# Kernel optimization log

Measured on AMD Instinct MI355X. Metric: run time of the kernel, lower is better.

## Reference

```python
import jax, jax.numpy as jnp
import numpy as np

D_MODEL = 2048
MLP = 8192
E = 8
R = 16
ALPHA = 32
SCALING = ALPHA / R  # lora_alpha / rank


def setup_inputs() -> dict:
    key = jax.random.key(0)
    ks = jax.random.split(key, 16)
    s = 0.02
    return {
        "x": jax.random.normal(ks[0], (4, 1024, D_MODEL), dtype=jnp.float32),
        # frozen base weights (nn.Linear stores [out, in])
        "w_gate": jax.random.normal(ks[1], (MLP, D_MODEL), dtype=jnp.float32) * s,
        "w_up": jax.random.normal(ks[2], (MLP, D_MODEL), dtype=jnp.float32) * s,
        "w_down": jax.random.normal(ks[3], (D_MODEL, MLP), dtype=jnp.float32) * s,
        # router
        "router_w": jax.random.normal(ks[4], (E, D_MODEL), dtype=jnp.float32) * s,
        "router_b": jnp.zeros((E,), dtype=jnp.float32),
        # LoRA expert params: A [E, r, fan_in], B [E, fan_out, r]
        "A_gate": jax.random.normal(ks[5], (E, R, D_MODEL), dtype=jnp.float32) * s,
        "B_gate": jax.random.normal(ks[6], (E, MLP, R), dtype=jnp.float32) * s,
        "A_up": jax.random.normal(ks[7], (E, R, D_MODEL), dtype=jnp.float32) * s,
        "B_up": jax.random.normal(ks[8], (E, MLP, R), dtype=jnp.float32) * s,
        "A_down": jax.random.normal(ks[9], (E, R, MLP), dtype=jnp.float32) * s,
        "B_down": jax.random.normal(ks[10], (E, D_MODEL, R), dtype=jnp.float32) * s,
    }


def _lora_moe_sparse(inp, W, A, B, onehot):
    # inp: [B,S,din], W: [dout,din], A: [E,r,din], B: [E,dout,r], onehot: [B,S,E]
    base = jnp.einsum("bsd,od->bso", inp, W)
    # low-rank projection for every expert is tiny: [B,S,E,r]
    t = jnp.einsum("bsd,erd->bser", inp, A)
    # top-1 dispatch: onehot zeroes out non-selected experts (== scatter assign,
    # since each token has exactly one expert)
    lora = jnp.einsum("bser,bse,eor->bso", t, onehot, B) * SCALING
    return base + lora


def reference(x, w_gate, w_up, w_down, router_w, router_b,
              A_gate, B_gate, A_up, B_up, A_down, B_down):
    logits = jnp.einsum("bsd,ed->bse", x, router_w) + router_b
    routing = jax.nn.softmax(logits, axis=-1)
    index = jnp.argmax(routing, axis=-1)                 # [B,S]
    y_hard = jax.nn.one_hot(index, E, dtype=logits.dtype)  # [B,S,E]
    expert_choice = y_hard - jax.lax.stop_gradient(routing) + routing

    gate_out = _lora_moe_sparse(x, w_gate, A_gate, B_gate, y_hard)
    up_out = _lora_moe_sparse(x, w_up, A_up, B_up, y_hard)
    h = jax.nn.silu(gate_out) * up_out
    out = _lora_moe_sparse(h, w_down, A_down, B_down, y_hard)
    return (out, routing, expert_choice)
```

## Files before the change

kernel.cpp:

```cpp
#include <hip/hip_runtime.h>
#include <stdint.h>

#define NTOK   4096
#define DM     2048
#define DMLP   8192
#define NEXP   8
#define NRANK  16
#define SCAL   2.0f

#define LDXA 2304
#define LDHA 8320

typedef __bf16 bf16x8 __attribute__((ext_vector_type(8)));
typedef float  f32x4  __attribute__((ext_vector_type(4)));
typedef unsigned short u16;

__device__ __forceinline__ u16 f2bf(float f) {
  unsigned u = __float_as_uint(f);
  u += 0x7fffu + ((u >> 16) & 1u);
  return (u16)(u >> 16);
}

__device__ __forceinline__ void gload_lds16(const void* g, void* l) {
  __builtin_amdgcn_global_load_lds((const __attribute__((address_space(1))) void*)g,
                                   (__attribute__((address_space(3))) void*)l, 16, 0, 0);
}

__global__ void prep_kernel(const float* __restrict__ wg, const float* __restrict__ wu,
                            const float* __restrict__ wd,
                            const float* __restrict__ Ag, const float* __restrict__ Au,
                            const float* __restrict__ Ad,
                            const float* __restrict__ Bg, const float* __restrict__ Bu,
                            const float* __restrict__ Bd,
                            u16* __restrict__ wgx, u16* __restrict__ wux,
                            u16* __restrict__ wdx, u16* __restrict__ Aab,
                            u16* __restrict__ Adb) {
  const int gt = blockIdx.x * blockDim.x + threadIdx.x;
  const int gs = gridDim.x * blockDim.x;

  for (int i = gt; i < DMLP * 512; i += gs) {
    const int o = i >> 9, c = (i & 511) << 2;
    float4 v = ((const float4*)wg)[i];
    ushort4 ov; ov.x = f2bf(v.x); ov.y = f2bf(v.y); ov.z = f2bf(v.z); ov.w = f2bf(v.w);
    *(ushort4*)(wgx + (size_t)o * LDXA + c) = ov;
    v = ((const float4*)wu)[i];
    ov.x = f2bf(v.x); ov.y = f2bf(v.y); ov.z = f2bf(v.z); ov.w = f2bf(v.w);
    *(ushort4*)(wux + (size_t)o * LDXA + c) = ov;
  }
  for (int i = gt; i < DM * 2048; i += gs) {
    const int o = i >> 11, c = (i & 2047) << 2;
    float4 v = ((const float4*)wd)[i];
    ushort4 ov; ov.x = f2bf(v.x); ov.y = f2bf(v.y); ov.z = f2bf(v.z); ov.w = f2bf(v.w);
    *(ushort4*)(wdx + (size_t)o * LDHA + c) = ov;
  }
  for (int i = gt; i < 256 * 512; i += gs) {
    float4 v = (i < 128 * 512) ? ((const float4*)Ag)[i] : ((const float4*)Au)[i - 128 * 512];
    ushort4 ov; ov.x = f2bf(v.x); ov.y = f2bf(v.y); ov.z = f2bf(v.z); ov.w = f2bf(v.w);
    ((ushort4*)Aab)[i] = ov;
  }
  for (int i = gt; i < 128 * 2048; i += gs) {
    float4 v = ((const float4*)Ad)[i];
    ushort4 ov; ov.x = f2bf(v.x); ov.y = f2bf(v.y); ov.z = f2bf(v.z); ov.w = f2bf(v.w);
    ((ushort4*)Adb)[i] = ov;
  }
  for (int i = gt; i < DMLP * 256; i += gs) {
    const int o = i >> 8, c = i & 255;
    const int e = (c & 127) >> 4, r = c & 15;
    u16 vg = 0, vu = 0;
    if (c < 128) vg = f2bf(Bg[((size_t)e * DMLP + o) * NRANK + r]);
    else         vu = f2bf(Bu[((size_t)e * DMLP + o) * NRANK + r]);
    wgx[(size_t)o * LDXA + 2048 + c] = vg;
    wux[(size_t)o * LDXA + 2048 + c] = vu;
  }
  for (int i = gt; i < DM * 128; i += gs) {
    const int o = i >> 7, c = i & 127;
    const int e = c >> 4, r = c & 15;
    wdx[(size_t)o * LDHA + 8192 + c] = f2bf(Bd[((size_t)e * DM + o) * NRANK + r]);
  }
}

__global__ void router_kernel(const float* __restrict__ x,
                              const float* __restrict__ rw,
                              const float* __restrict__ rb,
                              u16* __restrict__ xa,
                              int* __restrict__ idx,
                              float* __restrict__ out_rout,
                              float* __restrict__ out_ec) {
  const int wave = threadIdx.x >> 6;
  const int lane = threadIdx.x & 63;
  const int m = blockIdx.x * 4 + wave;

  const float4* xrow = (const float4*)(x + (size_t)m * DM + lane * 32);
  float4 xv[8];
#pragma unroll
  for (int i = 0; i < 8; ++i) xv[i] = xrow[i];

  uint4 o[4];
  unsigned* op = (unsigned*)o;
#pragma unroll
  for (int i = 0; i < 8; ++i) {
    op[2*i]   = (unsigned)f2bf(xv[i].x) | ((unsigned)f2bf(xv[i].y) << 16);
    op[2*i+1] = (unsigned)f2bf(xv[i].z) | ((unsigned)f2bf(xv[i].w) << 16);
  }
  uint4* xdst = (uint4*)(xa + (size_t)m * LDXA + lane * 32);
#pragma unroll
  for (int i = 0; i < 4; ++i) xdst[i] = o[i];

  float lg[NEXP];
#pragma unroll
  for (int e = 0; e < NEXP; ++e) {
    const float4* wrow = (const float4*)(rw + (size_t)e * DM + lane * 32);
    float s = 0.f;
#pragma unroll
    for (int i = 0; i < 8; ++i) {
      float4 wv = wrow[i];
      s += xv[i].x*wv.x + xv[i].y*wv.y + xv[i].z*wv.z + xv[i].w*wv.w;
    }
#pragma unroll
    for (int off = 32; off > 0; off >>= 1) s += __shfl_xor(s, off, 64);
    lg[e] = s + rb[e];
  }

  float mx = lg[0];
#pragma unroll
  for (int e = 1; e < NEXP; ++e) mx = fmaxf(mx, lg[e]);
  float ex[NEXP], se = 0.f;
#pragma unroll
  for (int e = 0; e < NEXP; ++e) { ex[e] = expf(lg[e] - mx); se += ex[e]; }
  float inv = 1.f / se;
  int best = 0; float bv = lg[0];
#pragma unroll
  for (int e = 1; e < NEXP; ++e) if (lg[e] > bv) { bv = lg[e]; best = e; }

  if (lane == 0) {
    idx[m] = best;
#pragma unroll
    for (int e = 0; e < NEXP; ++e) {
      float r = ex[e] * inv;
      out_rout[(size_t)m * NEXP + e] = r;
      float hard = (e == best) ? 1.f : 0.f;
      out_ec[(size_t)m * NEXP + e] = (hard - r) + r;
    }
  }
}

template<int MODE>
__global__ __launch_bounds__(256, 2)
void gemm_kernel(const u16* __restrict__ A,
                 const u16* __restrict__ B0,
                 const int* __restrict__ idx,
                 void* __restrict__ Cout)
{
  constexpr int LDA = (MODE == 0) ? LDXA : LDHA;
  constexpr int LDB = (MODE == 0) ? 2048 : 8192;
  constexpr int NKI = (MODE == 0) ? 64 : 32;

  __shared__ u16 lds[16384];

  const int tid = threadIdx.x;
  const int w = tid >> 6;
  const int l = tid & 63;
  const int wm = w >> 1, wn = w & 1;
  const int mtile = blockIdx.x;
  const int ntile = (MODE == 3) ? 0 : (int)blockIdx.y;
  const int ks    = (MODE == 3) ? (int)blockIdx.y : 0;
  const int kb0   = (MODE == 3) ? ks * 1024 : 0;

  int srow[2];
  srow[0] = w * 16 + (l >> 2);
  srow[1] = 64 + srow[0];
  const int chunk = (l & 3) ^ ((srow[0] >> 1) & 3);
  const int scol = chunk * 8;

  const u16* aptr[2];
  const u16* bptr[2];
#pragma unroll
  for (int i = 0; i < 2; ++i) {
    aptr[i] = A + (size_t)(mtile * 128 + srow[i]) * LDA + kb0 + scol;
    bptr[i] = B0 + (size_t)(ntile * 128 + srow[i]) * LDB + kb0 + scol;
  }

  char* ldsc = (char*)lds;
  auto stage = [&](int buf, int kt) {
    const int kk = kt * 32;
    char* base = ldsc + buf * 16384;
#pragma unroll
    for (int i = 0; i < 2; ++i) {
      gload_lds16(aptr[i] + kk, base + i * 4096 + w * 1024);
      gload_lds16(bptr[i] + kk, base + 8192 + i * 4096 + w * 1024);
    }
  };

  f32x4 acc[4][4];
  f32x4 zf = {0.f, 0.f, 0.f, 0.f};
#pragma unroll
  for (int a = 0; a < 4; ++a)
#pragma unroll
    for (int b = 0; b < 4; ++b) acc[a][b] = zf;

  stage(0, 0);
  __syncthreads();

  const int kq   = l >> 4;
  const int arow = wm * 64 + (l & 15);
  const int brow = wn * 64 + (l & 15);
  const int axor = (kq ^ ((arow >> 1) & 3)) << 4;
  const int bxor = (kq ^ ((brow >> 1) & 3)) << 4;

  for (int kt = 0; kt < NKI; ++kt) {
    const int buf = kt & 1;
    if (kt + 1 < NKI) stage(buf ^ 1, kt + 1);
    const char* bA = ldsc + buf * 16384;
    const char* bB = bA + 8192;
    bf16x8 af[4], bfr[4];
#pragma unroll
    for (int fm = 0; fm < 4; ++fm)
      af[fm] = *(const bf16x8*)(bA + (arow + fm * 16) * 64 + axor);
#pragma unroll
    for (int fn = 0; fn < 4; ++fn)
      bfr[fn] = *(const bf16x8*)(bB + (brow + fn * 16) * 64 + bxor);
#pragma unroll
    for (int fm = 0; fm < 4; ++fm)
#pragma unroll
      for (int fn = 0; fn < 4; ++fn)
        acc[fm][fn] = __builtin_amdgcn_mfma_f32_16x16x32_bf16(af[fm], bfr[fn], acc[fm][fn], 0, 0, 0);
    __syncthreads();
  }

  const int lq = l >> 4;
  const int lr = l & 15;

  if (MODE == 0) {
    u16* X = (u16*)Cout;
#pragma unroll
    for (int fm = 0; fm < 4; ++fm)
#pragma unroll
      for (int fn = 0; fn < 4; ++fn)
        for (int j = 0; j < 4; ++j) {
          int m = mtile * 128 + wm * 64 + fm * 16 + lq * 4 + j;
          int c = ntile * 128 + wn * 64 + fn * 16 + lr;
          int e = idx[m];
          u16 v = (((c & 127) >> 4) == e) ? f2bf(SCAL * acc[fm][fn][j]) : (u16)0;
          X[(size_t)m * LDXA + 2048 + c] = v;
        }
  } else {
    float* P = (float*)Cout + (size_t)ks * NTOK * 128;
#pragma unroll
    for (int fm = 0; fm < 4; ++fm)
#pragma unroll
      for (int fn = 0; fn < 4; ++fn)
        for (int j = 0; j < 4; ++j) {
          int m = mtile * 128 + wm * 64 + fm * 16 + lq * 4 + j;
          int c = wn * 64 + fn * 16 + lr;
          P[(size_t)m * 128 + c] = acc[fm][fn][j];
        }
  }
}

__global__ __launch_bounds__(512, 2)
void gemm_gu(const u16* __restrict__ Ag,
             const u16* __restrict__ B0g,
             const u16* __restrict__ B1g,
             u16* __restrict__ H)
{
  constexpr int NKT = 36;
  __shared__ char L[131072];

  const int tid = threadIdx.x, w = tid >> 6, l = tid & 63;
  const int wm = w >> 2, wn = w & 3;
  const int bid = blockIdx.x;
  const int rr = bid >> 3;
  const int mtile = rr >> 3;
  const int ntile = (bid & 7) * 8 + (rr & 7);

  const u16 *agb0, *agb1, *bgb0, *bgb1;
  {
    int row0 = tid >> 2, row1 = 128 + row0;
    int lc = (tid & 3) ^ ((row0 >> 1) & 3);
    agb0 = Ag + (size_t)(mtile * 256 + row0) * LDXA + lc * 8;
    agb1 = Ag + (size_t)(mtile * 256 + row1) * LDXA + lc * 8;
    int c0 = ntile * 128 + ((row0 >> 5) << 4) + (row0 & 15);
    int c1 = ntile * 128 + ((row1 >> 5) << 4) + (row1 & 15);
    bgb0 = (((row0 >> 4) & 1) ? B1g : B0g) + (size_t)c0 * LDXA + lc * 8;
    bgb1 = (((row1 >> 4) & 1) ? B1g : B0g) + (size_t)c1 * LDXA + lc * 8;
  }
  const int sdst = w * 1024;

#define STGA(z, kt) { const int ko_ = ((kt) < NKT ? (kt) : NKT - 1) * 64 + ((z) & 1) * 32; \
    gload_lds16(agb0 + ko_, L + (z) * 16384 + sdst); \
    gload_lds16(agb1 + ko_, L + (z) * 16384 + 8192 + sdst); }
#define STGB(z, kt) { const int ko_ = ((kt) < NKT ? (kt) : NKT - 1) * 64 + ((z) & 1) * 32; \
    gload_lds16(bgb0 + ko_, L + 65536 + (z) * 16384 + sdst); \
    gload_lds16(bgb1 + ko_, L + 65536 + (z) * 16384 + 8192 + sdst); }

  const int lr = l & 15;
  const int kob = (((l >> 4) ^ ((lr >> 1) & 3)) << 4);
  const int abase = (wm * 128 + lr) * 64 + kob;
  const int bbase = (wn * 64 + lr) * 64 + kob;

  bf16x8 A0_[4], A1_[4], B0_[4], B1_[4];
#define RDA(S, z, qa) _Pragma("unroll") for (int f = 0; f < 4; ++f) \
    S[f] = *(const bf16x8*)(L + (z) * 16384 + abase + (qa) * 4096 + f * 1024);
#define RDB(S, z) _Pragma("unroll") for (int f = 0; f < 4; ++f) \
    S[f] = *(const bf16x8*)(L + 65536 + (z) * 16384 + bbase + f * 1024);

  f32x4 acc[8][4];
  f32x4 zf = {0.f, 0.f, 0.f, 0.f};
#pragma unroll
  for (int a = 0; a < 8; ++a)
#pragma unroll
    for (int b = 0; b < 4; ++b) acc[a][b] = zf;

#define MF(qa, AS, BS) \
  __builtin_amdgcn_s_setprio(1); \
  _Pragma("unroll") for (int f = 0; f < 4; ++f) \
    _Pragma("unroll") for (int n = 0; n < 4; ++n) \
      acc[(qa) * 4 + f][n] = __builtin_amdgcn_mfma_f32_16x16x32_bf16(AS[f], BS[n], acc[(qa) * 4 + f][n], 0, 0, 0); \
  __builtin_amdgcn_s_setprio(0);

#define VMW  { asm volatile("s_waitcnt vmcnt(6)" ::: "memory"); __builtin_amdgcn_sched_barrier(0); }
#define PEND { __builtin_amdgcn_sched_barrier(0); __builtin_amdgcn_s_barrier(); __builtin_amdgcn_sched_barrier(0); }

  STGA(0, 0) STGB(0, 0)
  STGA(1, 0) STGB(1, 0)
  STGA(2, 1) STGB(2, 1)
  VMW
  PEND
  RDB(B0_, 0) RDA(A0_, 0, 0)

  for (int it = 0; it < NKT / 2; ++it) {
    const int k1 = 2 * it + 1, k2 = 2 * it + 2, k3 = 2 * it + 3;
    STGA(3, k1)
    RDA(A1_, 0, 1)
    MF(0, A0_, B0_)  VMW  PEND
    STGB(3, k1)
    RDB(B1_, 1) RDA(A0_, 1, 0)
    MF(1, A1_, B0_)  PEND
    STGA(0, k2)
    RDA(A1_, 1, 1)
    MF(0, A0_, B1_)  VMW  PEND
    STGB(0, k2)
    RDB(B0_, 2) RDA(A0_, 2, 0)
    MF(1, A1_, B1_)  PEND
    STGA(1, k2)
    RDA(A1_, 2, 1)
    MF(0, A0_, B0_)  VMW  PEND
    STGB(1, k2)
    RDB(B1_, 3) RDA(A0_, 3, 0)
    MF(1, A1_, B0_)  PEND
    STGA(2, k3)
    RDA(A1_, 3, 1)
    MF(0, A0_, B1_)  VMW  PEND
    STGB(2, k3)
    RDB(B0_, 0) RDA(A0_, 0, 0)
    MF(1, A1_, B1_)  PEND
  }

  const int lq = l >> 4;
#pragma unroll
  for (int fm = 0; fm < 8; ++fm)
    for (int jj = 0; jj < 4; ++jj) {
      const int m = mtile * 256 + wm * 128 + fm * 16 + lq * 4 + jj;
#pragma unroll
      for (int p = 0; p < 2; ++p) {
        float g = acc[fm][2 * p][jj];
        float u = acc[fm][2 * p + 1][jj];
        float e = __builtin_amdgcn_exp2f(g * -1.44269504089f);
        float h = g * __builtin_amdgcn_rcpf(1.f + e) * u;
        const int c = ntile * 128 + (wn * 2 + p) * 16 + lr;
        H[(size_t)m * LDHA + c] = f2bf(h);
      }
    }
#undef RDA
#undef RDB
#undef MF
#undef STGA
#undef STGB
#undef VMW
#undef PEND
}

__global__ __launch_bounds__(512, 2)
void gemm6(const u16* __restrict__ Ag,
           const u16* __restrict__ Bg,
           float* __restrict__ C)
{
  __shared__ char L[147456];
  const int tid = threadIdx.x, w = tid >> 6, l = tid & 63;
  const int wm = w >> 2, wn = w & 3;
  const int bid = blockIdx.x;
  const int swz = (bid & 7) * 32 + (bid >> 3);
  const int mtile = swz >> 3;
  const int ntile = swz & 7;

  const u16 *agb0, *bgb0, *bgb1;
  {
    int row0 = tid >> 2;
    int lc = (tid & 3) ^ ((row0 >> 1) & 3);
    agb0 = Ag + (size_t)(mtile * 128 + row0) * LDHA + lc * 8;
    bgb0 = Bg + (size_t)(ntile * 256 + row0) * LDHA + lc * 8;
    bgb1 = Bg + (size_t)(ntile * 256 + 128 + row0) * LDHA + lc * 8;
  }
  const int sdst = w * 1024;

#define STG6(z, g) { const int gg_ = (g) < 260 ? (g) : 259; \
    const int ko_ = (gg_ >> 1) * 64 + (gg_ & 1) * 32; \
    gload_lds16(agb0 + ko_, L + (z) * 24576 + sdst); \
    gload_lds16(bgb0 + ko_, L + (z) * 24576 + 8192 + sdst); \
    gload_lds16(bgb1 + ko_, L + (z) * 24576 + 16384 + sdst); }

  const int lr = l & 15;
  const int kob = (((l >> 4) ^ ((lr >> 1) & 3)) << 4);
  const int abase = (wm * 64 + lr) * 64 + kob;
  const int bbase = (wn * 64 + lr) * 64 + kob;

  bf16x8 A0_[4], A1_[4], B0_[4], B1_[4];
#define RDA6(S, z) _Pragma("unroll") for (int f = 0; f < 4; ++f) \
    S[f] = *(const bf16x8*)(L + (z) * 24576 + abase + f * 1024);
#define RDB6(S, z) _Pragma("unroll") for (int f = 0; f < 4; ++f) \
    S[f] = *(const bf16x8*)(L + (z) * 24576 + 8192 + bbase + f * 1024);

  f32x4 acc[4][4];
  f32x4 zf = {0.f, 0.f, 0.f, 0.f};
#pragma unroll
  for (int a = 0; a < 4; ++a)
#pragma unroll
    for (int b = 0; b < 4; ++b) acc[a][b] = zf;

#define MF6(AS, BS) \
  __builtin_amdgcn_s_setprio(1); \
  _Pragma("unroll") for (int f = 0; f < 4; ++f) \
    _Pragma("unroll") for (int n = 0; n < 4; ++n) \
      acc[f][n] = __builtin_amdgcn_mfma_f32_16x16x32_bf16(AS[f], BS[n], acc[f][n], 0, 0, 0); \
  __builtin_amdgcn_s_setprio(0);

#define VMW6 { asm volatile("s_waitcnt vmcnt(6)" ::: "memory"); __builtin_amdgcn_sched_barrier(0); }
#define PEND6 { __builtin_amdgcn_sched_barrier(0); __builtin_amdgcn_s_barrier(); __builtin_amdgcn_sched_barrier(0); }

  STG6(0, 0) STG6(1, 1) STG6(2, 2) STG6(3, 3)
  VMW6
  PEND6
  RDB6(B0_, 0) RDA6(A0_, 0)

  for (int it = 0; it < 43; ++it) {
    const int g4 = it * 6 + 4;
    STG6(4, g4)      RDB6(B1_, 1) RDA6(A1_, 1)  MF6(A0_, B0_)  VMW6  PEND6
    STG6(5, g4 + 1)  RDB6(B0_, 2) RDA6(A0_, 2)  MF6(A1_, B1_)  VMW6  PEND6
    STG6(0, g4 + 2)  RDB6(B1_, 3) RDA6(A1_, 3)  MF6(A0_, B0_)  VMW6  PEND6
    STG6(1, g4 + 3)  RDB6(B0_, 4) RDA6(A0_, 4)  MF6(A1_, B1_)  VMW6  PEND6
    STG6(2, g4 + 4)  RDB6(B1_, 5) RDA6(A1_, 5)  MF6(A0_, B0_)  VMW6  PEND6
    STG6(3, g4 + 5)  RDB6(B0_, 0) RDA6(A0_, 0)  MF6(A1_, B1_)  VMW6  PEND6
  }
  RDB6(B1_, 1) RDA6(A1_, 1)
  MF6(A0_, B0_)
  MF6(A1_, B1_)

  const int lq = l >> 4;
#pragma unroll
  for (int fm = 0; fm < 4; ++fm)
#pragma unroll
    for (int n = 0; n < 4; ++n)
      for (int jj = 0; jj < 4; ++jj) {
        const int m = mtile * 128 + wm * 64 + fm * 16 + lq * 4 + jj;
        const int c = ntile * 256 + wn * 64 + n * 16 + lr;
        C[(size_t)m * DM + c] = acc[fm][n][jj];
      }
#undef RDA6
#undef RDB6
#undef MF6
#undef STG6
#undef VMW6
#undef PEND6
}

__global__ void td_reduce(const float* __restrict__ part,
                          const int* __restrict__ idx,
                          u16* __restrict__ ha) {
  int i = blockIdx.x * blockDim.x + threadIdx.x;
  int m = i >> 7, c = i & 127;
  float s = 0.f;
#pragma unroll
  for (int k = 0; k < 8; ++k) s += part[(size_t)k * NTOK * 128 + i];
  u16 v = ((c >> 4) == idx[m]) ? f2bf(SCAL * s) : (u16)0;
  ha[(size_t)m * LDHA + 8192 + c] = v;
}

extern "C" void kernel_launch(void* const* d_in, const int* in_sizes, int n_in,
                              void* d_out, int out_size, void* d_ws, size_t ws_size,
                              hipStream_t stream) {
  const float* x  = (const float*)d_in[0];
  const float* wg = (const float*)d_in[1];
  const float* wu = (const float*)d_in[2];
  const float* wd = (const float*)d_in[3];
  const float* rw = (const float*)d_in[4];
  const float* rb = (const float*)d_in[5];
  const float* Ag = (const float*)d_in[6];
  const float* Bg = (const float*)d_in[7];
  const float* Au = (const float*)d_in[8];
  const float* Bu = (const float*)d_in[9];
  const float* Ad = (const float*)d_in[10];
  const float* Bd = (const float*)d_in[11];

  float* out      = (float*)d_out;
  float* out_rout = out + (size_t)NTOK * DM;
  float* out_ec   = out_rout + (size_t)NTOK * NEXP;

  char* ws = (char*)d_ws;
  size_t off = 0;
  auto take = [&](size_t b) { void* p = ws + off; off += (b + 255) & ~(size_t)255; return p; };
  u16*   xa   = (u16*)take((size_t)NTOK * LDXA * 2);
  u16*   ha   = (u16*)take((size_t)NTOK * LDHA * 2);
  u16*   wgx  = (u16*)take((size_t)DMLP * LDXA * 2);
  u16*   wux  = (u16*)take((size_t)DMLP * LDXA * 2);
  u16*   wdx  = (u16*)take((size_t)DM * LDHA * 2);
  u16*   Aab  = (u16*)take((size_t)256 * DM * 2);
  u16*   Adb  = (u16*)take((size_t)128 * DMLP * 2);
  float* tdp  = (float*)take((size_t)8 * NTOK * 128 * 4);
  int*   idx  = (int*)take((size_t)NTOK * 4);
  if (off > ws_size) return;

  prep_kernel<<<2048, 256, 0, stream>>>(wg, wu, wd, Ag, Au, Ad, Bg, Bu, Bd,
                                        wgx, wux, wdx, Aab, Adb);

  router_kernel<<<NTOK / 4, 256, 0, stream>>>(x, rw, rb, xa, idx, out_rout, out_ec);

  gemm_kernel<0><<<dim3(32, 2), 256, 0, stream>>>(xa, Aab, idx, xa);
  gemm_gu<<<1024, 512, 0, stream>>>(xa, wgx, wux, ha);
  gemm_kernel<3><<<dim3(32, 8), 256, 0, stream>>>(ha, Adb, idx, tdp);
  td_reduce<<<NTOK * 128 / 256, 256, 0, stream>>>(tdp, idx, ha);
  gemm6<<<256, 512, 0, stream>>>(ha, wdx, out);
}
```

Before: 556.7 us.

## Restructure gate/up GEMM pipeline into per-slice stages with fewer barriers

The gate/up fused GEMM main loop is reorganised. It now stages A and B for a whole 32-wide k-slice together in one buffer and runs 32 MFMAs per phase, instead of splitting A and B loads across half-phases of 16 MFMAs. The aim is to halve the number of block barriers per k-step and give the scheduler larger MFMA groups to overlap with LDS reads and global loads. In exchange it uses more A fragment registers, which adds register pressure at two blocks per CU, and it changes the vmcnt wait depth.

```diff
diff --git a/kernel.cpp b/kernel.cpp
--- a/kernel.cpp
+++ b/kernel.cpp
@@ -263,7 +263,7 @@
              const u16* __restrict__ B1g,
              u16* __restrict__ H)
 {
-  constexpr int NKT = 36;
+  constexpr int NSL = 72;
   __shared__ char L[131072];
 
   const int tid = threadIdx.x, w = tid >> 6, l = tid & 63;
@@ -286,10 +286,9 @@
   }
   const int sdst = w * 1024;
 
-#define STGA(z, kt) { const int ko_ = ((kt) < NKT ? (kt) : NKT - 1) * 64 + ((z) & 1) * 32; \
+#define STG(z, s) { const int ko_ = ((s) < NSL ? (s) : NSL - 1) * 32; \
     gload_lds16(agb0 + ko_, L + (z) * 16384 + sdst); \
-    gload_lds16(agb1 + ko_, L + (z) * 16384 + 8192 + sdst); }
-#define STGB(z, kt) { const int ko_ = ((kt) < NKT ? (kt) : NKT - 1) * 64 + ((z) & 1) * 32; \
+    gload_lds16(agb1 + ko_, L + (z) * 16384 + 8192 + sdst); \
     gload_lds16(bgb0 + ko_, L + 65536 + (z) * 16384 + sdst); \
     gload_lds16(bgb1 + ko_, L + 65536 + (z) * 16384 + 8192 + sdst); }
 
@@ -298,9 +297,9 @@
   const int abase = (wm * 128 + lr) * 64 + kob;
   const int bbase = (wn * 64 + lr) * 64 + kob;
 
-  bf16x8 A0_[4], A1_[4], B0_[4], B1_[4];
-#define RDA(S, z, qa) _Pragma("unroll") for (int f = 0; f < 4; ++f) \
-    S[f] = *(const bf16x8*)(L + (z) * 16384 + abase + (qa) * 4096 + f * 1024);
+  bf16x8 A0_[8], A1_[8], B0_[4], B1_[4];
+#define RDA8(S, z) _Pragma("unroll") for (int f = 0; f < 8; ++f) \
+    S[f] = *(const bf16x8*)(L + (z) * 16384 + abase + (f >> 2) * 4096 + (f & 3) * 1024);
 #define RDB(S, z) _Pragma("unroll") for (int f = 0; f < 4; ++f) \
     S[f] = *(const bf16x8*)(L + 65536 + (z) * 16384 + bbase + f * 1024);
 
@@ -311,49 +310,35 @@
 #pragma unroll
     for (int b = 0; b < 4; ++b) acc[a][b] = zf;
 
-#define MF(qa, AS, BS) \
+#define MF32(AS, BS) \
   __builtin_amdgcn_s_setprio(1); \
-  _Pragma("unroll") for (int f = 0; f < 4; ++f) \
+  _Pragma("unroll") for (int f = 0; f < 8; ++f) \
     _Pragma("unroll") for (int n = 0; n < 4; ++n) \
-      acc[(qa) * 4 + f][n] = __builtin_amdgcn_mfma_f32_16x16x32_bf16(AS[f], BS[n], acc[(qa) * 4 + f][n], 0, 0, 0); \
+      acc[f][n] = __builtin_amdgcn_mfma_f32_16x16x32_bf16(AS[f], BS[n], acc[f][n], 0, 0, 0); \
   __builtin_amdgcn_s_setprio(0);
 
-#define VMW  { asm volatile("s_waitcnt vmcnt(6)" ::: "memory"); __builtin_amdgcn_sched_barrier(0); }
+#define VMW  { asm volatile("s_waitcnt vmcnt(4)" ::: "memory"); __builtin_amdgcn_sched_barrier(0); }
 #define PEND { __builtin_amdgcn_sched_barrier(0); __builtin_amdgcn_s_barrier(); __builtin_amdgcn_sched_barrier(0); }
 
-  STGA(0, 0) STGB(0, 0)
-  STGA(1, 0) STGB(1, 0)
-  STGA(2, 1) STGB(2, 1)
+  STG(0, 0) STG(1, 1) STG(2, 2)
   VMW
   PEND
-  RDB(B0_, 0) RDA(A0_, 0, 0)
-
-  for (int it = 0; it < NKT / 2; ++it) {
-    const int k1 = 2 * it + 1, k2 = 2 * it + 2, k3 = 2 * it + 3;
-    STGA(3, k1)
-    RDA(A1_, 0, 1)
-    MF(0, A0_, B0_)  VMW  PEND
-    STGB(3, k1)
-    RDB(B1_, 1) RDA(A0_, 1, 0)
-    MF(1, A1_, B0_)  PEND
-    STGA(0, k2)
-    RDA(A1_, 1, 1)
-    MF(0, A0_, B1_)  VMW  PEND
-    STGB(0, k2)
-    RDB(B0_, 2) RDA(A0_, 2, 0)
-    MF(1, A1_, B1_)  PEND
-    STGA(1, k2)
-    RDA(A1_, 2, 1)
-    MF(0, A0_, B0_)  VMW  PEND
-    STGB(1, k2)
-    RDB(B1_, 3) RDA(A0_, 3, 0)
-    MF(1, A1_, B0_)  PEND
-    STGA(2, k3)
-    RDA(A1_, 3, 1)
-    MF(0, A0_, B1_)  VMW  PEND
-    STGB(2, k3)
-    RDB(B0_, 0) RDA(A0_, 0, 0)
-    MF(1, A1_, B1_)  PEND
+  RDB(B0_, 0) RDA8(A0_, 0)
+
+  for (int it = 0; it < NSL / 4; ++it) {
+    const int s = 4 * it;
+    STG(3, s + 3)
+    RDB(B1_, 1) RDA8(A1_, 1)
+    MF32(A0_, B0_)  VMW  PEND
+    STG(0, s + 4)
+    RDB(B0_, 2) RDA8(A0_, 2)
+    MF32(A1_, B1_)  VMW  PEND
+    STG(1, s + 5)
+    RDB(B1_, 3) RDA8(A1_, 3)
+    MF32(A0_, B0_)  VMW  PEND
+    STG(2, s + 6)
+    RDB(B0_, 0) RDA8(A0_, 0)
+    MF32(A1_, B1_)  VMW  PEND
   }
 
   const int lq = l >> 4;
@@ -371,11 +356,10 @@
         H[(size_t)m * LDHA + c] = f2bf(h);
       }
     }
-#undef RDA
+#undef RDA8
 #undef RDB
-#undef MF
-#undef STGA
-#undef STGB
+#undef MF32
+#undef STG
 #undef VMW
 #undef PEND
 }
```

Result: slower. 604.0 us (+8.5%).

## Overlap big weight conversion with LoRA-A GEMM and merge router with small prep

Applied to the files above, without the earlier changes.

The router and the small LoRA-A conversions are merged into one kernel. The large fp32-to-bf16 conversion of the base and LoRA-B weights is moved into the same launch as the x·A GEMM: the first 64 blocks run the GEMM and the remaining blocks grid-stride over the weight conversion. This removes two launches and lets the narrow 64-block GEMM overlap with bandwidth-bound conversion work instead of leaving most CUs idle. The risk is that conversion blocks compete for bandwidth with the GEMM blocks and slow them down.

```diff
diff --git a/kernel.cpp b/kernel.cpp
--- a/kernel.cpp
+++ b/kernel.cpp
@@ -26,17 +26,190 @@
                                    (__attribute__((address_space(3))) void*)l, 16, 0, 0);
 }
 
-__global__ void prep_kernel(const float* __restrict__ wg, const float* __restrict__ wu,
-                            const float* __restrict__ wd,
-                            const float* __restrict__ Ag, const float* __restrict__ Au,
-                            const float* __restrict__ Ad,
-                            const float* __restrict__ Bg, const float* __restrict__ Bu,
-                            const float* __restrict__ Bd,
-                            u16* __restrict__ wgx, u16* __restrict__ wux,
-                            u16* __restrict__ wdx, u16* __restrict__ Aab,
-                            u16* __restrict__ Adb) {
+__global__ void prep_small(const float* __restrict__ x,
+                           const float* __restrict__ rw,
+                           const float* __restrict__ rb,
+                           u16* __restrict__ xa,
+                           int* __restrict__ idx,
+                           float* __restrict__ out_rout,
+                           float* __restrict__ out_ec,
+                           const float* __restrict__ Ag,
+                           const float* __restrict__ Au,
+                           const float* __restrict__ Ad,
+                           u16* __restrict__ Aab,
+                           u16* __restrict__ Adb) {
+  const int wave = threadIdx.x >> 6;
+  const int lane = threadIdx.x & 63;
+  const int m = blockIdx.x * 4 + wave;
+
+  const float4* xrow = (const float4*)(x + (size_t)m * DM + lane * 32);
+  float4 xv[8];
+#pragma unroll
+  for (int i = 0; i < 8; ++i) xv[i] = xrow[i];
+
+  uint4 o[4];
+  unsigned* op = (unsigned*)o;
+#pragma unroll
+  for (int i = 0; i < 8; ++i) {
+    op[2*i]   = (unsigned)f2bf(xv[i].x) | ((unsigned)f2bf(xv[i].y) << 16);
+    op[2*i+1] = (unsigned)f2bf(xv[i].z) | ((unsigned)f2bf(xv[i].w) << 16);
+  }
+  uint4* xdst = (uint4*)(xa + (size_t)m * LDXA + lane * 32);
+#pragma unroll
+  for (int i = 0; i < 4; ++i) xdst[i] = o[i];
+
+  float lg[NEXP];
+#pragma unroll
+  for (int e = 0; e < NEXP; ++e) {
+    const float4* wrow = (const float4*)(rw + (size_t)e * DM + lane * 32);
+    float s = 0.f;
+#pragma unroll
+    for (int i = 0; i < 8; ++i) {
+      float4 wv = wrow[i];
+      s += xv[i].x*wv.x + xv[i].y*wv.y + xv[i].z*wv.z + xv[i].w*wv.w;
+    }
+#pragma unroll
+    for (int off = 32; off > 0; off >>= 1) s += __shfl_xor(s, off, 64);
+    lg[e] = s + rb[e];
+  }
+
+  float mx = lg[0];
+#pragma unroll
+  for (int e = 1; e < NEXP; ++e) mx = fmaxf(mx, lg[e]);
+  float ex[NEXP], se = 0.f;
+#pragma unroll
+  for (int e = 0; e < NEXP; ++e) { ex[e] = expf(lg[e] - mx); se += ex[e]; }
+  float inv = 1.f / se;
+  int best = 0; float bv = lg[0];
+#pragma unroll
+  for (int e = 1; e < NEXP; ++e) if (lg[e] > bv) { bv = lg[e]; best = e; }
+
+  if (lane == 0) {
+    idx[m] = best;
+#pragma unroll
+    for (int e = 0; e < NEXP; ++e) {
+      float r = ex[e] * inv;
+      out_rout[(size_t)m * NEXP + e] = r;
+      float hard = (e == best) ? 1.f : 0.f;
+      out_ec[(size_t)m * NEXP + e] = (hard - r) + r;
+    }
+  }
+
   const int gt = blockIdx.x * blockDim.x + threadIdx.x;
   const int gs = gridDim.x * blockDim.x;
+  for (int i = gt; i < 256 * 512; i += gs) {
+    float4 v = (i < 128 * 512) ? ((const float4*)Ag)[i] : ((const float4*)Au)[i - 128 * 512];
+    ushort4 ov; ov.x = f2bf(v.x); ov.y = f2bf(v.y); ov.z = f2bf(v.z); ov.w = f2bf(v.w);
+    ((ushort4*)Aab)[i] = ov;
+  }
+  for (int i = gt; i < 128 * 2048; i += gs) {
+    float4 v = ((const float4*)Ad)[i];
+    ushort4 ov; ov.x = f2bf(v.x); ov.y = f2bf(v.y); ov.z = f2bf(v.z); ov.w = f2bf(v.w);
+    ((ushort4*)Adb)[i] = ov;
+  }
+}
+
+__global__ __launch_bounds__(256, 2)
+void gemm0_prep(const u16* __restrict__ A,
+                const u16* __restrict__ B0,
+                const int* __restrict__ idx,
+                u16* __restrict__ Xout,
+                const float* __restrict__ wg, const float* __restrict__ wu,
+                const float* __restrict__ wd,
+                const float* __restrict__ Bg, const float* __restrict__ Bu,
+                const float* __restrict__ Bd,
+                u16* __restrict__ wgx, u16* __restrict__ wux,
+                u16* __restrict__ wdx)
+{
+  __shared__ u16 lds[16384];
+
+  if (blockIdx.x < 64) {
+    const int tid = threadIdx.x;
+    const int w = tid >> 6;
+    const int l = tid & 63;
+    const int wm = w >> 1, wn = w & 1;
+    const int mtile = (int)blockIdx.x >> 1;
+    const int ntile = (int)blockIdx.x & 1;
+
+    int srow[2];
+    srow[0] = w * 16 + (l >> 2);
+    srow[1] = 64 + srow[0];
+    const int chunk = (l & 3) ^ ((srow[0] >> 1) & 3);
+    const int scol = chunk * 8;
+
+    const u16* aptr[2];
+    const u16* bptr[2];
+#pragma unroll
+    for (int i = 0; i < 2; ++i) {
+      aptr[i] = A + (size_t)(mtile * 128 + srow[i]) * LDXA + scol;
+      bptr[i] = B0 + (size_t)(ntile * 128 + srow[i]) * 2048 + scol;
+    }
+
+    char* ldsc = (char*)lds;
+    auto stage = [&](int buf, int kt) {
+      const int kk = kt * 32;
+      char* base = ldsc + buf * 16384;
+#pragma unroll
+      for (int i = 0; i < 2; ++i) {
+        gload_lds16(aptr[i] + kk, base + i * 4096 + w * 1024);
+        gload_lds16(bptr[i] + kk, base + 8192 + i * 4096 + w * 1024);
+      }
+    };
+
+    f32x4 acc[4][4];
+    f32x4 zf = {0.f, 0.f, 0.f, 0.f};
+#pragma unroll
+    for (int a = 0; a < 4; ++a)
+#pragma unroll
+      for (int b = 0; b < 4; ++b) acc[a][b] = zf;
+
+    stage(0, 0);
+    __syncthreads();
+
+    const int kq   = l >> 4;
+    const int arow = wm * 64 + (l & 15);
+    const int brow = wn * 64 + (l & 15);
+    const int axor = (kq ^ ((arow >> 1) & 3)) << 4;
+    const int bxor = (kq ^ ((brow >> 1) & 3)) << 4;
+
+    for (int kt = 0; kt < 64; ++kt) {
+      const int buf = kt & 1;
+      if (kt + 1 < 64) stage(buf ^ 1, kt + 1);
+      const char* bA = ldsc + buf * 16384;
+      const char* bB = bA + 8192;
+      bf16x8 af[4], bfr[4];
+#pragma unroll
+      for (int fm = 0; fm < 4; ++fm)
+        af[fm] = *(const bf16x8*)(bA + (arow + fm * 16) * 64 + axor);
+#pragma unroll
+      for (int fn = 0; fn < 4; ++fn)
+        bfr[fn] = *(const bf16x8*)(bB + (brow + fn * 16) * 64 + bxor);
+#pragma unroll
+      for (int fm = 0; fm < 4; ++fm)
+#pragma unroll
+        for (int fn = 0; fn < 4; ++fn)
+          acc[fm][fn] = __builtin_amdgcn_mfma_f32_16x16x32_bf16(af[fm], bfr[fn], acc[fm][fn], 0, 0, 0);
+      __syncthreads();
+    }
+
+    const int lq = l >> 4;
+    const int lr = l & 15;
+#pragma unroll
+    for (int fm = 0; fm < 4; ++fm)
+#pragma unroll
+      for (int fn = 0; fn < 4; ++fn)
+        for (int j = 0; j < 4; ++j) {
+          int m = mtile * 128 + wm * 64 + fm * 16 + lq * 4 + j;
+          int c = ntile * 128 + wn * 64 + fn * 16 + lr;
+          int e = idx[m];
+          u16 v = (((c & 127) >> 4) == e) ? f2bf(SCAL * acc[fm][fn][j]) : (u16)0;
+          Xout[(size_t)m * LDXA + 2048 + c] = v;
+        }
+    return;
+  }
+
+  const int gt = ((int)blockIdx.x - 64) * blockDim.x + threadIdx.x;
+  const int gs = ((int)gridDim.x - 64) * blockDim.x;
 
   for (int i = gt; i < DMLP * 512; i += gs) {
     const int o = i >> 9, c = (i & 511) << 2;
@@ -53,16 +226,6 @@
     ushort4 ov; ov.x = f2bf(v.x); ov.y = f2bf(v.y); ov.z = f2bf(v.z); ov.w = f2bf(v.w);
     *(ushort4*)(wdx + (size_t)o * LDHA + c) = ov;
   }
-  for (int i = gt; i < 256 * 512; i += gs) {
-    float4 v = (i < 128 * 512) ? ((const float4*)Ag)[i] : ((const float4*)Au)[i - 128 * 512];
-    ushort4 ov; ov.x = f2bf(v.x); ov.y = f2bf(v.y); ov.z = f2bf(v.z); ov.w = f2bf(v.w);
-    ((ushort4*)Aab)[i] = ov;
-  }
-  for (int i = gt; i < 128 * 2048; i += gs) {
-    float4 v = ((const float4*)Ad)[i];
-    ushort4 ov; ov.x = f2bf(v.x); ov.y = f2bf(v.y); ov.z = f2bf(v.z); ov.w = f2bf(v.w);
-    ((ushort4*)Adb)[i] = ov;
-  }
   for (int i = gt; i < DMLP * 256; i += gs) {
     const int o = i >> 8, c = i & 255;
     const int e = (c & 127) >> 4, r = c & 15;
@@ -79,82 +242,11 @@
   }
 }
 
-__global__ void router_kernel(const float* __restrict__ x,
-                              const float* __restrict__ rw,
-                              const float* __restrict__ rb,
-                              u16* __restrict__ xa,
-                              int* __restrict__ idx,
-                              float* __restrict__ out_rout,
-                              float* __restrict__ out_ec) {
-  const int wave = threadIdx.x >> 6;
-  const int lane = threadIdx.x & 63;
-  const int m = blockIdx.x * 4 + wave;
-
-  const float4* xrow = (const float4*)(x + (size_t)m * DM + lane * 32);
-  float4 xv[8];
-#pragma unroll
-  for (int i = 0; i < 8; ++i) xv[i] = xrow[i];
-
-  uint4 o[4];
-  unsigned* op = (unsigned*)o;
-#pragma unroll
-  for (int i = 0; i < 8; ++i) {
-    op[2*i]   = (unsigned)f2bf(xv[i].x) | ((unsigned)f2bf(xv[i].y) << 16);
-    op[2*i+1] = (unsigned)f2bf(xv[i].z) | ((unsigned)f2bf(xv[i].w) << 16);
-  }
-  uint4* xdst = (uint4*)(xa + (size_t)m * LDXA + lane * 32);
-#pragma unroll
-  for (int i = 0; i < 4; ++i) xdst[i] = o[i];
-
-  float lg[NEXP];
-#pragma unroll
-  for (int e = 0; e < NEXP; ++e) {
-    const float4* wrow = (const float4*)(rw + (size_t)e * DM + lane * 32);
-    float s = 0.f;
-#pragma unroll
-    for (int i = 0; i < 8; ++i) {
-      float4 wv = wrow[i];
-      s += xv[i].x*wv.x + xv[i].y*wv.y + xv[i].z*wv.z + xv[i].w*wv.w;
-    }
-#pragma unroll
-    for (int off = 32; off > 0; off >>= 1) s += __shfl_xor(s, off, 64);
-    lg[e] = s + rb[e];
-  }
-
-  float mx = lg[0];
-#pragma unroll
-  for (int e = 1; e < NEXP; ++e) mx = fmaxf(mx, lg[e]);
-  float ex[NEXP], se = 0.f;
-#pragma unroll
-  for (int e = 0; e < NEXP; ++e) { ex[e] = expf(lg[e] - mx); se += ex[e]; }
-  float inv = 1.f / se;
-  int best = 0; float bv = lg[0];
-#pragma unroll
-  for (int e = 1; e < NEXP; ++e) if (lg[e] > bv) { bv = lg[e]; best = e; }
-
-  if (lane == 0) {
-    idx[m] = best;
-#pragma unroll
-    for (int e = 0; e < NEXP; ++e) {
-      float r = ex[e] * inv;
-      out_rout[(size_t)m * NEXP + e] = r;
-      float hard = (e == best) ? 1.f : 0.f;
-      out_ec[(size_t)m * NEXP + e] = (hard - r) + r;
-    }
-  }
-}
-
-template<int MODE>
 __global__ __launch_bounds__(256, 2)
-void gemm_kernel(const u16* __restrict__ A,
-                 const u16* __restrict__ B0,
-                 const int* __restrict__ idx,
-                 void* __restrict__ Cout)
+void gemm3_kernel(const u16* __restrict__ A,
+                  const u16* __restrict__ B0,
+                  void* __restrict__ Cout)
 {
-  constexpr int LDA = (MODE == 0) ? LDXA : LDHA;
-  constexpr int LDB = (MODE == 0) ? 2048 : 8192;
-  constexpr int NKI = (MODE == 0) ? 64 : 32;
-
   __shared__ u16 lds[16384];
 
   const int tid = threadIdx.x;
@@ -162,9 +254,8 @@
   const int l = tid & 63;
   const int wm = w >> 1, wn = w & 1;
   const int mtile = blockIdx.x;
-  const int ntile = (MODE == 3) ? 0 : (int)blockIdx.y;
-  const int ks    = (MODE == 3) ? (int)blockIdx.y : 0;
-  const int kb0   = (MODE == 3) ? ks * 1024 : 0;
+  const int ks    = (int)blockIdx.y;
+  const int kb0   = ks * 1024;
 
   int srow[2];
   srow[0] = w * 16 + (l >> 2);
@@ -176,8 +267,8 @@
   const u16* bptr[2];
 #pragma unroll
   for (int i = 0; i < 2; ++i) {
-    aptr[i] = A + (size_t)(mtile * 128 + srow[i]) * LDA + kb0 + scol;
-    bptr[i] = B0 + (size_t)(ntile * 128 + srow[i]) * LDB + kb0 + scol;
+    aptr[i] = A + (size_t)(mtile * 128 + srow[i]) * LDHA + kb0 + scol;
+    bptr[i] = B0 + (size_t)srow[i] * 8192 + kb0 + scol;
   }
 
   char* ldsc = (char*)lds;
@@ -207,9 +298,9 @@
   const int axor = (kq ^ ((arow >> 1) & 3)) << 4;
   const int bxor = (kq ^ ((brow >> 1) & 3)) << 4;
 
-  for (int kt = 0; kt < NKI; ++kt) {
+  for (int kt = 0; kt < 32; ++kt) {
     const int buf = kt & 1;
-    if (kt + 1 < NKI) stage(buf ^ 1, kt + 1);
+    if (kt + 1 < 32) stage(buf ^ 1, kt + 1);
     const char* bA = ldsc + buf * 16384;
     const char* bB = bA + 8192;
     bf16x8 af[4], bfr[4];
@@ -229,32 +320,16 @@
 
   const int lq = l >> 4;
   const int lr = l & 15;
-
-  if (MODE == 0) {
-    u16* X = (u16*)Cout;
-#pragma unroll
-    for (int fm = 0; fm < 4; ++fm)
-#pragma unroll
-      for (int fn = 0; fn < 4; ++fn)
-        for (int j = 0; j < 4; ++j) {
-          int m = mtile * 128 + wm * 64 + fm * 16 + lq * 4 + j;
-          int c = ntile * 128 + wn * 64 + fn * 16 + lr;
-          int e = idx[m];
-          u16 v = (((c & 127) >> 4) == e) ? f2bf(SCAL * acc[fm][fn][j]) : (u16)0;
-          X[(size_t)m * LDXA + 2048 + c] = v;
-        }
-  } else {
-    float* P = (float*)Cout + (size_t)ks * NTOK * 128;
-#pragma unroll
-    for (int fm = 0; fm < 4; ++fm)
-#pragma unroll
-      for (int fn = 0; fn < 4; ++fn)
-        for (int j = 0; j < 4; ++j) {
-          int m = mtile * 128 + wm * 64 + fm * 16 + lq * 4 + j;
-          int c = wn * 64 + fn * 16 + lr;
-          P[(size_t)m * 128 + c] = acc[fm][fn][j];
-        }
-  }
+  float* P = (float*)Cout + (size_t)ks * NTOK * 128;
+#pragma unroll
+  for (int fm = 0; fm < 4; ++fm)
+#pragma unroll
+    for (int fn = 0; fn < 4; ++fn)
+      for (int j = 0; j < 4; ++j) {
+        int m = mtile * 128 + wm * 64 + fm * 16 + lq * 4 + j;
+        int c = wn * 64 + fn * 16 + lr;
+        P[(size_t)m * 128 + c] = acc[fm][fn][j];
+      }
 }
 
 __global__ __launch_bounds__(512, 2)
@@ -519,14 +594,12 @@
   int*   idx  = (int*)take((size_t)NTOK * 4);
   if (off > ws_size) return;
 
-  prep_kernel<<<2048, 256, 0, stream>>>(wg, wu, wd, Ag, Au, Ad, Bg, Bu, Bd,
-                                        wgx, wux, wdx, Aab, Adb);
-
-  router_kernel<<<NTOK / 4, 256, 0, stream>>>(x, rw, rb, xa, idx, out_rout, out_ec);
-
-  gemm_kernel<0><<<dim3(32, 2), 256, 0, stream>>>(xa, Aab, idx, xa);
+  prep_small<<<NTOK / 4, 256, 0, stream>>>(x, rw, rb, xa, idx, out_rout, out_ec,
+                                           Ag, Au, Ad, Aab, Adb);
+  gemm0_prep<<<2112, 256, 0, stream>>>(xa, Aab, idx, xa,
+                                       wg, wu, wd, Bg, Bu, Bd, wgx, wux, wdx);
   gemm_gu<<<1024, 512, 0, stream>>>(xa, wgx, wux, ha);
-  gemm_kernel<3><<<dim3(32, 8), 256, 0, stream>>>(ha, Adb, idx, tdp);
+  gemm3_kernel<<<dim3(32, 8), 256, 0, stream>>>(ha, Adb, tdp);
   td_reduce<<<NTOK * 128 / 256, 256, 0, stream>>>(tdp, idx, ha);
   gemm6<<<256, 512, 0, stream>>>(ha, wdx, out);
 }
```

New measurement: 540.5 us. -2.9%, faster.
